# Kernel optimization log

Hardware: AMD Instinct MI355X
Metric: run time of the kernel (lower is better)

## Reference

```python
import jax, jax.numpy as jnp
import numpy as np

D_MODEL = 1024
N_HEADS = 8
D_HEAD = 64
D_FF = 4096
LAMBDA_INIT = 0.8
EPS = 1e-5


def _ln(x, g, b):
    m = jnp.mean(x, axis=-1, keepdims=True)
    v = jnp.mean(jnp.square(x - m), axis=-1, keepdims=True)
    return (x - m) * jax.lax.rsqrt(v + EPS) * g + b


def setup_inputs() -> dict:
    key = jax.random.key(0)
    ks = jax.random.split(key, 24)
    D, H, Dh, F = D_MODEL, N_HEADS, D_HEAD, D_FF
    P = 2 * H * Dh  # projection width for q/k/v (== D here)
    s = lambda fan: 1.0 / np.sqrt(fan)
    inp = {
        'x': jax.random.normal(ks[0], (2, 2048, D), jnp.float32),
        'ln1_g': jnp.ones((D,), jnp.float32), 'ln1_b': jnp.zeros((D,), jnp.float32),
        'ln2_g': jnp.ones((D,), jnp.float32), 'ln2_b': jnp.zeros((D,), jnp.float32),
        'Wq': jax.random.normal(ks[1], (D, P), jnp.float32) * s(D), 'bq': jnp.zeros((P,), jnp.float32),
        'Wk': jax.random.normal(ks[2], (D, P), jnp.float32) * s(D), 'bk': jnp.zeros((P,), jnp.float32),
        'Wv': jax.random.normal(ks[3], (D, P), jnp.float32) * s(D), 'bv': jnp.zeros((P,), jnp.float32),
        'Wo': jax.random.normal(ks[4], (P, D), jnp.float32) * s(P), 'bo': jnp.zeros((D,), jnp.float32),
        'lq1': jax.random.normal(ks[5], (H, Dh), jnp.float32) * 0.1,
        'lk1': jax.random.normal(ks[6], (H, Dh), jnp.float32) * 0.1,
        'lq2': jax.random.normal(ks[7], (H, Dh), jnp.float32) * 0.1,
        'lk2': jax.random.normal(ks[8], (H, Dh), jnp.float32) * 0.1,
        'gn_w': jnp.ones((P,), jnp.float32), 'gn_b': jnp.zeros((P,), jnp.float32),
        'W1': jax.random.normal(ks[9], (D, F), jnp.float32) * s(D), 'b1': jnp.zeros((F,), jnp.float32),
        'Wg': jax.random.normal(ks[10], (F, F), jnp.float32) * s(F), 'bg': jnp.zeros((F,), jnp.float32),
        'W2': jax.random.normal(ks[11], (F, D), jnp.float32) * s(F), 'b2': jnp.zeros((D,), jnp.float32),
    }
    return inp


def reference(x, ln1_g, ln1_b, ln2_g, ln2_b, Wq, bq, Wk, bk, Wv, bv, Wo, bo,
              lq1, lk1, lq2, lk2, gn_w, gn_b, W1, b1, Wg, bg, W2, b2):
    B, S, D = x.shape
    H, Dh = N_HEADS, D_HEAD
    scale = 1.0 / np.sqrt(Dh)

    # --- differential attention sublayer (pre-norm) ---
    h = _ln(x, ln1_g, ln1_b)
    q = (h @ Wq + bq).reshape(B, S, H, 2, Dh)
    k = (h @ Wk + bk).reshape(B, S, H, 2, Dh)
    v = (h @ Wv + bv).reshape(B, S, H, 2 * Dh)

    A1 = jax.nn.softmax(jnp.einsum('bshd,bthd->bhst', q[..., 0, :], k[..., 0, :]) * scale, axis=-1)
    A2 = jax.nn.softmax(jnp.einsum('bshd,bthd->bhst', q[..., 1, :], k[..., 1, :]) * scale, axis=-1)

    lam = (jnp.exp(jnp.sum(lq1 * lk1, axis=-1))
           - jnp.exp(jnp.sum(lq2 * lk2, axis=-1)) + LAMBDA_INIT)  # [H]
    diff = A1 - lam[None, :, None, None] * A2                     # [B,H,S,S]
    o = jnp.einsum('bhst,bthe->bshe', diff, v)                    # [B,S,H,2*Dh]

    # headwise GroupNorm over the 2*Dh channels of each head
    mu = jnp.mean(o, axis=-1, keepdims=True)
    var = jnp.mean(jnp.square(o - mu), axis=-1, keepdims=True)
    o = (o - mu) * jax.lax.rsqrt(var + EPS)
    o = o * gn_w.reshape(H, 2 * Dh) + gn_b.reshape(H, 2 * Dh)
    o = o * (1.0 - LAMBDA_INIT)

    attn_out = o.reshape(B, S, 2 * H * Dh) @ Wo + bo
    x = x + attn_out

    # --- FFN sublayer: note source applies prenorm2 BEFORE residual split ---
    x = _ln(x, ln2_g, ln2_b)
    u = x @ W1 + b1
    u = u * jax.nn.silu(u @ Wg + bg)   # swiGLU gate
    return x + (u @ W2 + b2)
```

## Files before the change

kernel.cpp:

```cpp
#include <hip/hip_runtime.h>
#include <hip/hip_bf16.h>


typedef __attribute__((ext_vector_type(8))) __bf16 bf16x8;
typedef __attribute__((ext_vector_type(4))) float f32x4;

#define GAS __attribute__((address_space(1)))
#define LAS __attribute__((address_space(3)))

__device__ __forceinline__ unsigned short f2bf(float f) {
  unsigned u = __float_as_uint(f);
  u += 0x7fffu + ((u >> 16) & 1u);
  return (unsigned short)(u >> 16);
}
__device__ __forceinline__ float bf2f(unsigned short s) {
  return __uint_as_float(((unsigned)s) << 16);
}

__global__ __launch_bounds__(256)
void transpose_cvt(const float* __restrict__ W, unsigned short* __restrict__ WT,
                   int K, int N, float scale) {
  __shared__ float tile[64][65];
  const int n0 = blockIdx.x * 64, k0 = blockIdx.y * 64;
  const int tr = threadIdx.x >> 4, tc = (threadIdx.x & 15) * 4;
#pragma unroll
  for (int i = 0; i < 4; ++i) {
    const float4 v = *(const float4*)&W[(size_t)(k0 + tr + i * 16) * N + n0 + tc];
    tile[tr + i * 16][tc + 0] = v.x;
    tile[tr + i * 16][tc + 1] = v.y;
    tile[tr + i * 16][tc + 2] = v.z;
    tile[tr + i * 16][tc + 3] = v.w;
  }
  __syncthreads();
#pragma unroll
  for (int i = 0; i < 4; ++i) {
    const int n = tr + i * 16;
    ushort4 o;
    o.x = f2bf(tile[tc + 0][n] * scale);
    o.y = f2bf(tile[tc + 1][n] * scale);
    o.z = f2bf(tile[tc + 2][n] * scale);
    o.w = f2bf(tile[tc + 3][n] * scale);
    *(ushort4*)&WT[(size_t)(n0 + n) * K + k0 + tc] = o;
  }
}

__global__ void prep_bias(const float* __restrict__ bq, const float* __restrict__ bk,
                          const float* __restrict__ bv, float* __restrict__ out,
                          float qscale) {
  const int i = blockIdx.x * 256 + threadIdx.x;
  if (i < 1024) out[i] = bq[i] * qscale;
  else if (i < 2048) out[i] = bk[i - 1024];
  else out[i] = bv[i - 2048];
}

__global__ __launch_bounds__(256)
void k_pack(const unsigned short* __restrict__ qkv, unsigned short* __restrict__ KP) {
  const int bh = blockIdx.y, b = bh >> 3, h = bh & 7;
  const int s0 = blockIdx.x * 16;
  const int sl = threadIdx.x >> 4, e8 = (threadIdx.x & 15) * 8;
  const size_t src = (size_t)b * 2048 * 3072 + (size_t)(s0 + sl) * 3072 + 1024 + h * 128 + e8;
  const size_t dst = ((size_t)bh * 2048 + s0 + sl) * 128 + e8;
  *(uint4*)&KP[dst] = *(const uint4*)&qkv[src];
}

__global__ __launch_bounds__(256)
void v_transpose(const unsigned short* __restrict__ v, unsigned short* __restrict__ VT) {
  __shared__ unsigned short tile[64][65];
  const int s0 = blockIdx.x * 64, e0 = blockIdx.y * 64, bh = blockIdx.z;
  const int b = bh >> 3, h = bh & 7;
  const int tr = threadIdx.x >> 4, tc = (threadIdx.x & 15) * 4;
  const size_t inbase = (size_t)b * 2048 * 3072 + h * 128;
#pragma unroll
  for (int i = 0; i < 4; ++i) {
    const int r = tr + i * 16;
    const ushort4 val = *(const ushort4*)&v[inbase + (size_t)(s0 + r) * 3072 + e0 + tc];
    tile[r][tc + 0] = val.x;
    tile[r][tc + 1] = val.y;
    tile[r][tc + 2] = val.z;
    tile[r][tc + 3] = val.w;
  }
  __syncthreads();
#pragma unroll
  for (int i = 0; i < 4; ++i) {
    const int n = tr + i * 16;
    ushort4 oo;
    oo.x = tile[tc + 0][n];
    oo.y = tile[tc + 1][n];
    oo.z = tile[tc + 2][n];
    oo.w = tile[tc + 3][n];
    *(ushort4*)&VT[(size_t)(bh * 128 + e0 + n) * 2048 + s0 + tc] = oo;
  }
}

__global__ void lam_kernel(const float* __restrict__ lq1, const float* __restrict__ lk1,
                           const float* __restrict__ lq2, const float* __restrict__ lk2,
                           float* __restrict__ lam) {
  const int w = threadIdx.x >> 6, d = threadIdx.x & 63;
  float a = lq1[w * 64 + d] * lk1[w * 64 + d];
  float c = lq2[w * 64 + d] * lk2[w * 64 + d];
#pragma unroll
  for (int off = 32; off; off >>= 1) {
    a += __shfl_xor(a, off);
    c += __shfl_xor(c, off);
  }
  if (d == 0) lam[w] = __expf(a) - __expf(c) + 0.8f;
}

template <int WRITE_F32>
__global__ __launch_bounds__(256)
void ln_kernel(const float* __restrict__ x, const float* __restrict__ g,
               const float* __restrict__ bsh, unsigned short* __restrict__ obf,
               float* __restrict__ of32) {
  __shared__ float red[16];
  const int row = blockIdx.x, tid = threadIdx.x;
  const float4 v = *(const float4*)&x[(size_t)row * 1024 + tid * 4];
  float s = v.x + v.y + v.z + v.w;
  float q = v.x * v.x + v.y * v.y + v.z * v.z + v.w * v.w;
#pragma unroll
  for (int off = 32; off; off >>= 1) {
    s += __shfl_xor(s, off);
    q += __shfl_xor(q, off);
  }
  if ((tid & 63) == 0) {
    red[tid >> 6] = s;
    red[8 + (tid >> 6)] = q;
  }
  __syncthreads();
  s = red[0] + red[1] + red[2] + red[3];
  q = red[8] + red[9] + red[10] + red[11];
  const float mean = s * (1.f / 1024.f);
  const float var = q * (1.f / 1024.f) - mean * mean;
  const float rstd = rsqrtf(var + 1e-5f);
  const float4 gg = *(const float4*)&g[tid * 4];
  const float4 bb = *(const float4*)&bsh[tid * 4];
  float y0 = (v.x - mean) * rstd * gg.x + bb.x;
  float y1 = (v.y - mean) * rstd * gg.y + bb.y;
  float y2 = (v.z - mean) * rstd * gg.z + bb.z;
  float y3 = (v.w - mean) * rstd * gg.w + bb.w;
  const size_t base = (size_t)row * 1024 + tid * 4;
  ushort4 o;
  o.x = f2bf(y0); o.y = f2bf(y1); o.z = f2bf(y2); o.w = f2bf(y3);
  *(ushort4*)&obf[base] = o;
  if (WRITE_F32) {
    *(float4*)&of32[base] = make_float4(y0, y1, y2, y3);
  }
}

template <int EPI>
__global__ __launch_bounds__(256)
void gemm_n64(const unsigned short* __restrict__ A,
              const unsigned short* __restrict__ BT,
              const float* __restrict__ bias,
              const float* __restrict__ res,
              void* __restrict__ Cout, int M, int N, int K, float bscale) {
  __shared__ unsigned short ldsA[2][128 * 32];
  __shared__ unsigned short ldsB[2][64 * 32];
  const int tid = threadIdx.x;
  const int wv = tid >> 6, ln = tid & 63, lg = ln >> 4, lc = ln & 15;
  const int wm = wv >> 1, wn = wv & 1;
  const int nwg = gridDim.x * gridDim.y;
  const int linear = blockIdx.y * gridDim.x + blockIdx.x;
  const int swz = (linear & 7) * (nwg >> 3) + (linear >> 3);
  const int m0 = (swz / gridDim.x) * 128, n0 = (swz % gridDim.x) * 64;
  const int rsub = ln >> 2;
  const int sw_inner = ((ln & 3) * 16) ^ ((rsub & 3) << 4);
  const int acol = sw_inner >> 1;

  f32x4 acc[4][2];
#pragma unroll
  for (int i = 0; i < 4; ++i)
#pragma unroll
    for (int j = 0; j < 2; ++j) acc[i][j] = (f32x4)0.f;

  auto stage = [&](int buf, int k0) {
#pragma unroll
    for (int j = 0; j < 2; ++j) {
      const int rowblk = wv * 32 + j * 16;
      const unsigned short* ga = A + (size_t)(m0 + rowblk + rsub) * K + (k0 + acol);
      __builtin_amdgcn_global_load_lds((GAS void*)ga,
          (LAS void*)&ldsA[buf][rowblk * 32], 16, 0, 0);
    }
    const unsigned short* gb = BT + (size_t)(n0 + wv * 16 + rsub) * K + (k0 + acol);
    __builtin_amdgcn_global_load_lds((GAS void*)gb,
        (LAS void*)&ldsB[buf][wv * 16 * 32], 16, 0, 0);
  };

  const int nk = K / 32;
  stage(0, 0);
  int cur = 0;
  for (int i = 0; i < nk; ++i) {
    if (i + 1 < nk) {
      stage(cur ^ 1, (i + 1) * 32);
      asm volatile("s_waitcnt vmcnt(3)" ::: "memory");
    } else {
      asm volatile("s_waitcnt vmcnt(0)" ::: "memory");
    }
    __builtin_amdgcn_s_barrier();
    bf16x8 af[4], bf[2];
#pragma unroll
    for (int m = 0; m < 4; ++m) {
      const int r = wm * 64 + m * 16 + lc;
      af[m] = *(const bf16x8*)((const char*)&ldsA[cur][0] + r * 64 +
                               ((lg * 16) ^ ((r & 3) << 4)));
    }
#pragma unroll
    for (int n = 0; n < 2; ++n) {
      const int r = wn * 32 + n * 16 + lc;
      bf[n] = *(const bf16x8*)((const char*)&ldsB[cur][0] + r * 64 +
                               ((lg * 16) ^ ((r & 3) << 4)));
    }
    __builtin_amdgcn_s_setprio(1);
#pragma unroll
    for (int m = 0; m < 4; ++m)
#pragma unroll
      for (int n = 0; n < 2; ++n)
        acc[m][n] = __builtin_amdgcn_mfma_f32_16x16x32_bf16(af[m], bf[n], acc[m][n], 0, 0, 0);
    __builtin_amdgcn_s_setprio(0);
    __builtin_amdgcn_s_barrier();
    cur ^= 1;
  }

#pragma unroll
  for (int m = 0; m < 4; ++m) {
#pragma unroll
    for (int n = 0; n < 2; ++n) {
      const int c = n0 + wn * 32 + n * 16 + lc;
      const float bc = bias[c] * bscale;
#pragma unroll
      for (int j = 0; j < 4; ++j) {
        const int r = m0 + wm * 64 + m * 16 + lg * 4 + j;
        const size_t idx = (size_t)r * N + c;
        const float v = acc[m][n][j] + bc;
        if (EPI == 1) {
          ((float*)Cout)[idx] = res[idx] + v;
        } else {
          ((unsigned short*)Cout)[idx] = f2bf(v);
        }
      }
    }
  }
}

template <int EPI>
__global__ __launch_bounds__(512)
void gemm256(const unsigned short* __restrict__ A,
             const unsigned short* __restrict__ BT,
             const float* __restrict__ bias,
             const unsigned short* __restrict__ gate_u,
             unsigned short* __restrict__ Cout, int M, int N, int K) {
  __shared__ unsigned short lds[65536];
  const int tid = threadIdx.x;
  const int w = tid >> 6, ln = tid & 63, lg = ln >> 4, lc = ln & 15;
  const int wm = w >> 2, wn = w & 3;
  const int nwg = gridDim.x * gridDim.y;
  const int linear = blockIdx.y * gridDim.x + blockIdx.x;
  const int swzb = (linear & 7) * (nwg >> 3) + (linear >> 3);
  const int m0 = (swzb / gridDim.x) * 256, n0 = (swzb % gridDim.x) * 256;

  f32x4 acc[8][4];
#pragma unroll
  for (int i = 0; i < 8; ++i)
#pragma unroll
    for (int j = 0; j < 4; ++j) acc[i][j] = (f32x4)0.f;

  auto stage_half = [&](int tensor, int j, int hh) {
    const unsigned short* base = tensor ? BT : A;
    const int row0 = (tensor ? n0 : m0) + hh * 128;
    const int slot = tensor * 4 + (j & 1) * 2 + hh;
#pragma unroll
    for (int c = 0; c < 2; ++c) {
      const int chunk = w * 2 + c;
      const int L = chunk * 1024 + ln * 16;
      const int r = L >> 7, inner = L & 127;
      const char* src = (const char*)(base + (size_t)(row0 + r) * K + j * 64) +
                        (inner ^ ((r & 7) << 4));
      __builtin_amdgcn_global_load_lds((GAS void*)src,
          (LAS void*)((char*)lds + slot * 16384 + chunk * 1024), 16, 0, 0);
    }
  };
  auto read_a = [&](int j, int mf, int ks) -> bf16x8 {
    const int r = mf * 16 + lc;
    const int slot = (j & 1) * 2 + wm;
    const int cb = ks * 64 + lg * 16;
    return *(const bf16x8*)((const char*)lds + slot * 16384 + r * 128 +
                            (cb ^ ((r & 7) << 4)));
  };
  auto read_b = [&](int j, int nf, int ks) -> bf16x8 {
    const int R = wn * 64 + nf * 16 + lc;
    const int slot = 4 + (j & 1) * 2 + (R >> 7);
    const int r = R & 127;
    const int cb = ks * 64 + lg * 16;
    return *(const bf16x8*)((const char*)lds + slot * 16384 + r * 128 +
                            (cb ^ ((r & 7) << 4)));
  };

  const int nkt = K / 64;

  stage_half(0, 0, 0); stage_half(0, 0, 1);
  stage_half(1, 0, 0); stage_half(1, 0, 1);
  stage_half(1, 1, 0); stage_half(1, 1, 1);
  asm volatile("s_waitcnt vmcnt(0)" ::: "memory");
  __builtin_amdgcn_s_barrier();

  bf16x8 bfr[4][2];
  for (int it = 0; it < nkt / 2; ++it) {
    const int J = it * 2;
#pragma unroll
    for (int half = 0; half < 2; ++half) {
      const int jc = J + half;
#pragma unroll
      for (int q = 0; q < 4; ++q) {
        if (q == 0) {
#pragma unroll
          for (int nf = 0; nf < 4; ++nf)
#pragma unroll
            for (int ks = 0; ks < 2; ++ks) bfr[nf][ks] = read_b(jc, nf, ks);
        }
        bf16x8 afr[2][2];
#pragma unroll
        for (int mm = 0; mm < 2; ++mm)
#pragma unroll
          for (int ks = 0; ks < 2; ++ks) afr[mm][ks] = read_a(jc, q * 2 + mm, ks);
        if (half == 0) {
          if (q == 0) stage_half(0, J + 1, 0);
          if (q == 1) stage_half(0, J + 1, 1);
          if (q == 2 && J + 2 < nkt) stage_half(1, J + 2, 0);
          if (q == 3 && J + 2 < nkt) stage_half(1, J + 2, 1);
        } else {
          if (q == 0 && J + 2 < nkt) stage_half(0, J + 2, 0);
          if (q == 1 && J + 2 < nkt) stage_half(0, J + 2, 1);
          if (q == 2 && J + 3 < nkt) stage_half(1, J + 3, 0);
          if (q == 3 && J + 3 < nkt) stage_half(1, J + 3, 1);
        }
        if (q == 0) asm volatile("s_waitcnt lgkmcnt(8)" ::: "memory");
        __builtin_amdgcn_s_barrier();
        __builtin_amdgcn_s_setprio(1);
#pragma unroll
        for (int mm = 0; mm < 2; ++mm)
#pragma unroll
          for (int nf = 0; nf < 4; ++nf)
#pragma unroll
            for (int ks = 0; ks < 2; ++ks)
              acc[q * 2 + mm][nf] = __builtin_amdgcn_mfma_f32_16x16x32_bf16(
                  afr[mm][ks], bfr[nf][ks], acc[q * 2 + mm][nf], 0, 0, 0);
        __builtin_amdgcn_s_setprio(0);
        if (q == 3) asm volatile("s_waitcnt vmcnt(4)" ::: "memory");
        __builtin_amdgcn_s_barrier();
      }
    }
  }

#pragma unroll
  for (int mf = 0; mf < 8; ++mf) {
#pragma unroll
    for (int nf = 0; nf < 4; ++nf) {
      const int c = n0 + wn * 64 + nf * 16 + lc;
      const float bc = bias[c];
#pragma unroll
      for (int jj = 0; jj < 4; ++jj) {
        const int r = m0 + wm * 128 + mf * 16 + lg * 4 + jj;
        const size_t idx = (size_t)r * N + c;
        const float v = acc[mf][nf][jj] + bc;
        if (EPI == 0) {
          Cout[idx] = f2bf(v);
        } else {
          const float uu = bf2f(gate_u[idx]);
          const float sw = v / (1.f + __expf(-v));
          Cout[idx] = f2bf(uu * sw);
        }
      }
    }
  }
}

__global__ __launch_bounds__(256)
void attn_kernel(const unsigned short* __restrict__ q,
                 const unsigned short* __restrict__ KP,
                 const unsigned short* __restrict__ VT,
                 const float* __restrict__ lam,
                 const float* __restrict__ gn_w, const float* __restrict__ gn_b,
                 unsigned short* __restrict__ o) {
  constexpr int S = 2048;
  constexpr int QS = 3072;
  __shared__ unsigned short k_tile[2][32 * 128];
  __shared__ unsigned short v_tile[2][128 * 32];
  __shared__ unsigned short p_lds[4][2][512];
  const int tid = threadIdx.x, w = tid >> 6, ln = tid & 63, lg = ln >> 4, lc = ln & 15;
  const int id = blockIdx.x;
  const int bh = (id & 7) + 8 * ((id >> 8) & 1);
  const int qt = (id >> 3) & 31;
  const int h = bh & 7, b = bh >> 3;
  const size_t chan = (size_t)b * S * QS + h * 128;
  const size_t ochan = (size_t)b * S * 1024 + h * 128;
  const size_t kpbase = (size_t)bh * S * 128;
  const size_t vtbase = (size_t)bh * 128 * S;
  const int qrow = qt * 64 + w * 16 + lc;

  bf16x8 qf[2][2];
#pragma unroll
  for (int p = 0; p < 2; ++p)
#pragma unroll
    for (int ks = 0; ks < 2; ++ks)
      qf[p][ks] = *(const bf16x8*)&q[chan + (size_t)qrow * QS + p * 64 + ks * 32 + lg * 8];

  f32x4 O[2][8];
#pragma unroll
  for (int p = 0; p < 2; ++p)
#pragma unroll
    for (int ef = 0; ef < 8; ++ef) O[p][ef] = (f32x4)0.f;
  float lsum[2][4];
#pragma unroll
  for (int p = 0; p < 2; ++p)
#pragma unroll
    for (int j = 0; j < 4; ++j) lsum[p][j] = 0.f;

  const int prd = ((lc * 64 + lg * 16) ^ ((lc & 7) << 4)) >> 1;

  auto stage = [&](int buf, int t0) {
#pragma unroll
    for (int c = 0; c < 2; ++c) {
      {
        const int L = (w * 2 + c) * 1024 + ln * 16;
        const int r = L >> 8, inner = L & 255;
        const char* src = (const char*)(KP + kpbase + (size_t)(t0 + r) * 128) +
                          (inner ^ ((r & 7) << 4));
        __builtin_amdgcn_global_load_lds((GAS void*)src,
            (LAS void*)((char*)&k_tile[buf][0] + (w * 2 + c) * 1024), 16, 0, 0);
      }
      {
        const int L = (w * 2 + c) * 1024 + ln * 16;
        const int e = L >> 6, inner = L & 63;
        const char* src = (const char*)(VT + vtbase + (size_t)e * S + t0) +
                          (inner ^ ((e & 3) << 4));
        __builtin_amdgcn_global_load_lds((GAS void*)src,
            (LAS void*)((char*)&v_tile[buf][0] + (w * 2 + c) * 1024), 16, 0, 0);
      }
    }
  };

  auto compute = [&](int buf) {
    const char* kb = (const char*)&k_tile[buf][0];
    const char* vb = (const char*)&v_tile[buf][0];
    bf16x8 vf[8];
#pragma unroll
    for (int ef = 0; ef < 8; ++ef) {
      const int e = ef * 16 + lc;
      vf[ef] = *(const bf16x8*)(vb + e * 64 + ((lg * 16) ^ ((e & 3) << 4)));
    }
#pragma unroll
    for (int p = 0; p < 2; ++p) {
      bf16x8 kf[2][2];
#pragma unroll
      for (int tf = 0; tf < 2; ++tf) {
        const int r = tf * 16 + lc;
#pragma unroll
        for (int ks = 0; ks < 2; ++ks)
          kf[tf][ks] = *(const bf16x8*)(kb + r * 256 +
                          ((p * 128 + ks * 64 + lg * 16) ^ ((r & 7) << 4)));
      }
      f32x4 sfr[2];
      __builtin_amdgcn_s_setprio(1);
#pragma unroll
      for (int tf = 0; tf < 2; ++tf) {
        f32x4 acc = (f32x4)0.f;
#pragma unroll
        for (int ks = 0; ks < 2; ++ks)
          acc = __builtin_amdgcn_mfma_f32_16x16x32_bf16(qf[p][ks], kf[tf][ks], acc, 0, 0, 0);
        sfr[tf] = acc;
      }
      __builtin_amdgcn_s_setprio(0);

#pragma unroll
      for (int tf = 0; tf < 2; ++tf)
#pragma unroll
        for (int j = 0; j < 4; ++j) {
          const float e = __expf(sfr[tf][j]);
          lsum[p][j] += e;
          const int qq = lg * 4 + j;
          const int wi = ((qq * 64 + (tf * 16 + lc) * 2) ^ ((qq & 7) << 4)) >> 1;
          p_lds[w][p][wi] = f2bf(e);
        }

      const bf16x8 pa = *(const bf16x8*)&p_lds[w][p][prd];
      __builtin_amdgcn_s_setprio(1);
#pragma unroll
      for (int ef = 0; ef < 8; ++ef)
        O[p][ef] = __builtin_amdgcn_mfma_f32_16x16x32_bf16(pa, vf[ef], O[p][ef], 0, 0, 0);
      __builtin_amdgcn_s_setprio(0);
    }
  };

  stage(0, 0);
  int cur = 0;
  for (int it = 0; it < 64; ++it) {
    if (it < 63) {
      stage(cur ^ 1, (it + 1) * 32);
      asm volatile("s_waitcnt vmcnt(4)" ::: "memory");
    } else {
      asm volatile("s_waitcnt vmcnt(0)" ::: "memory");
    }
    __builtin_amdgcn_s_barrier();
    compute(cur);
    __builtin_amdgcn_s_barrier();
    cur ^= 1;
  }

#pragma unroll
  for (int p = 0; p < 2; ++p)
#pragma unroll
    for (int j = 0; j < 4; ++j) {
      float s = lsum[p][j];
      s += __shfl_xor(s, 1);
      s += __shfl_xor(s, 2);
      s += __shfl_xor(s, 4);
      s += __shfl_xor(s, 8);
      lsum[p][j] = s;
    }
  const float lamh = lam[h];
#pragma unroll
  for (int j = 0; j < 4; ++j) {
    const float inv1 = 1.f / lsum[0][j];
    const float inv2 = lamh / lsum[1][j];
    float dv[8], sum = 0.f, sq = 0.f;
#pragma unroll
    for (int ef = 0; ef < 8; ++ef) {
      dv[ef] = O[0][ef][j] * inv1 - O[1][ef][j] * inv2;
      sum += dv[ef];
      sq += dv[ef] * dv[ef];
    }
    sum += __shfl_xor(sum, 1); sq += __shfl_xor(sq, 1);
    sum += __shfl_xor(sum, 2); sq += __shfl_xor(sq, 2);
    sum += __shfl_xor(sum, 4); sq += __shfl_xor(sq, 4);
    sum += __shfl_xor(sum, 8); sq += __shfl_xor(sq, 8);
    const float mean = sum * (1.f / 128.f);
    const float var = sq * (1.f / 128.f) - mean * mean;
    const float rstd = rsqrtf(var + 1e-5f);
    const int row = qt * 64 + w * 16 + lg * 4 + j;
#pragma unroll
    for (int ef = 0; ef < 8; ++ef) {
      const int e = ef * 16 + lc;
      const float val = (dv[ef] - mean) * rstd * gn_w[h * 128 + e] + gn_b[h * 128 + e];
      o[ochan + (size_t)row * 1024 + e] = f2bf(val * 0.2f);
    }
  }
}

extern "C" void kernel_launch(void* const* d_in, const int* in_sizes, int n_in,
                              void* d_out, int out_size, void* d_ws, size_t ws_size,
                              hipStream_t stream) {
  (void)in_sizes; (void)n_in; (void)out_size; (void)ws_size;
  const float* x    = (const float*)d_in[0];
  const float* ln1g = (const float*)d_in[1];
  const float* ln1b = (const float*)d_in[2];
  const float* ln2g = (const float*)d_in[3];
  const float* ln2b = (const float*)d_in[4];
  const float* Wq   = (const float*)d_in[5];
  const float* bq   = (const float*)d_in[6];
  const float* Wk   = (const float*)d_in[7];
  const float* bk   = (const float*)d_in[8];
  const float* Wv   = (const float*)d_in[9];
  const float* bv   = (const float*)d_in[10];
  const float* Wo   = (const float*)d_in[11];
  const float* bo   = (const float*)d_in[12];
  const float* lq1  = (const float*)d_in[13];
  const float* lk1  = (const float*)d_in[14];
  const float* lq2  = (const float*)d_in[15];
  const float* lk2  = (const float*)d_in[16];
  const float* gnw  = (const float*)d_in[17];
  const float* gnb  = (const float*)d_in[18];
  const float* W1   = (const float*)d_in[19];
  const float* b1   = (const float*)d_in[20];
  const float* Wg   = (const float*)d_in[21];
  const float* bg   = (const float*)d_in[22];
  const float* W2   = (const float*)d_in[23];
  const float* b2   = (const float*)d_in[24];

  const int B = 2, S = 2048, D = 1024, F = 4096;
  const int M = B * S;
  const float qscale = 0.125f;

  char* ws = (char*)d_ws;
  size_t off = 0;
  auto alloc = [&](size_t bytes) {
    char* p = ws + off;
    off += (bytes + 255) & ~(size_t)255;
    return p;
  };
  unsigned short* WqkvT = (unsigned short*)alloc((size_t)3 * D * D * 2);
  unsigned short* WoT = (unsigned short*)alloc((size_t)D * D * 2);
  unsigned short* W1T = (unsigned short*)alloc((size_t)F * D * 2);
  unsigned short* WgT = (unsigned short*)alloc((size_t)F * F * 2);
  unsigned short* W2T = (unsigned short*)alloc((size_t)D * F * 2);
  float*          lamw= (float*)alloc(256);
  float*          bqkv= (float*)alloc(3072 * 4);
  unsigned short* h_bf= (unsigned short*)alloc((size_t)M * D * 2);
  unsigned short* qkv = (unsigned short*)alloc((size_t)M * 3 * D * 2);
  unsigned short* o_bf= (unsigned short*)alloc((size_t)M * D * 2);
  float*          x1  = (float*)alloc((size_t)M * D * 4);
  float*          x2  = (float*)alloc((size_t)M * D * 4);
  unsigned short* x2b = (unsigned short*)alloc((size_t)M * D * 2);
  unsigned short* u_bf= (unsigned short*)alloc((size_t)M * F * 2);
  unsigned short* w_bf= h_bf;

  unsigned short* KP = (unsigned short*)x1;
  unsigned short* VT = u_bf + (size_t)12 * 1024 * 1024;

  transpose_cvt<<<dim3(D / 64, D / 64), 256, 0, stream>>>(Wq, WqkvT, D, D, qscale);
  transpose_cvt<<<dim3(D / 64, D / 64), 256, 0, stream>>>(Wk, WqkvT + (size_t)D * D, D, D, 1.0f);
  transpose_cvt<<<dim3(D / 64, D / 64), 256, 0, stream>>>(Wv, WqkvT + (size_t)2 * D * D, D, D, 1.0f);
  transpose_cvt<<<dim3(D / 64, D / 64), 256, 0, stream>>>(Wo, WoT, D, D, 1.0f);
  transpose_cvt<<<dim3(F / 64, D / 64), 256, 0, stream>>>(W1, W1T, D, F, 1.0f);
  transpose_cvt<<<dim3(F / 64, F / 64), 256, 0, stream>>>(Wg, WgT, F, F, 1.0f);
  transpose_cvt<<<dim3(D / 64, F / 64), 256, 0, stream>>>(W2, W2T, F, D, 1.0f);
  prep_bias<<<12, 256, 0, stream>>>(bq, bk, bv, bqkv, qscale);
  lam_kernel<<<1, 512, 0, stream>>>(lq1, lk1, lq2, lk2, lamw);

  ln_kernel<0><<<M, 256, 0, stream>>>(x, ln1g, ln1b, h_bf, nullptr);
  gemm256<0><<<dim3(3 * D / 256, M / 256), 512, 0, stream>>>(h_bf, WqkvT, bqkv, nullptr, qkv, M, 3 * D, D);
  k_pack<<<dim3(S / 16, 16), 256, 0, stream>>>(qkv, KP);
  v_transpose<<<dim3(S / 64, 2, 16), 256, 0, stream>>>(qkv + 2048, VT);
  attn_kernel<<<dim3(512), 256, 0, stream>>>(qkv, KP, VT, lamw, gnw, gnb, o_bf);
  gemm_n64<1><<<dim3(D / 64, M / 128), 256, 0, stream>>>(o_bf, WoT, bo, x, x1, M, D, D, 1.0f);

  ln_kernel<1><<<M, 256, 0, stream>>>(x1, ln2g, ln2b, x2b, x2);
  gemm256<0><<<dim3(F / 256, M / 256), 512, 0, stream>>>(x2b, W1T, b1, nullptr, u_bf, M, F, D);
  gemm256<2><<<dim3(F / 256, M / 256), 512, 0, stream>>>(u_bf, WgT, bg, u_bf, w_bf, M, F, F);
  gemm_n64<1><<<dim3(D / 64, M / 128), 256, 0, stream>>>(w_bf, W2T, b2, x2, (float*)d_out, M, D, F, 1.0f);
}
```

Before: 451.6 us.

## Fuse K pack and V transpose, drop fp32 LN2 output, tune attention occupancy

Merges the K packing and V transpose kernels into one kv_prep launch that reads each QKV tile once. The second LayerNorm no longer writes an fp32 copy, and the final GEMM takes its residual from the bf16 normalized activations instead. This removes a launch and about 16MB of fp32 write and read traffic. It costs residual precision, because the final output now adds a bf16-rounded residual, and it adds launch_bounds(256,4) on the attention kernel, which may force register spills.

```diff
diff --git a/kernel.cpp b/kernel.cpp
--- a/kernel.cpp
+++ b/kernel.cpp
@@ -54,41 +54,38 @@
 }
 
 __global__ __launch_bounds__(256)
-void k_pack(const unsigned short* __restrict__ qkv, unsigned short* __restrict__ KP) {
+void kv_prep(const unsigned short* __restrict__ qkv, unsigned short* __restrict__ KP,
+             unsigned short* __restrict__ VT) {
+  __shared__ unsigned short tile[128][66];
   const int bh = blockIdx.y, b = bh >> 3, h = bh & 7;
-  const int s0 = blockIdx.x * 16;
-  const int sl = threadIdx.x >> 4, e8 = (threadIdx.x & 15) * 8;
-  const size_t src = (size_t)b * 2048 * 3072 + (size_t)(s0 + sl) * 3072 + 1024 + h * 128 + e8;
-  const size_t dst = ((size_t)bh * 2048 + s0 + sl) * 128 + e8;
-  *(uint4*)&KP[dst] = *(const uint4*)&qkv[src];
-}
-
-__global__ __launch_bounds__(256)
-void v_transpose(const unsigned short* __restrict__ v, unsigned short* __restrict__ VT) {
-  __shared__ unsigned short tile[64][65];
-  const int s0 = blockIdx.x * 64, e0 = blockIdx.y * 64, bh = blockIdx.z;
-  const int b = bh >> 3, h = bh & 7;
-  const int tr = threadIdx.x >> 4, tc = (threadIdx.x & 15) * 4;
+  const int s0 = blockIdx.x * 64;
   const size_t inbase = (size_t)b * 2048 * 3072 + h * 128;
+  const int tr = threadIdx.x >> 4, tc = (threadIdx.x & 15) * 8;
+#pragma unroll
+  for (int i = 0; i < 4; ++i) {
+    const int s = s0 + tr + i * 16;
+    *(uint4*)&KP[((size_t)bh * 2048 + s) * 128 + tc] =
+        *(const uint4*)&qkv[inbase + (size_t)s * 3072 + 1024 + tc];
+  }
 #pragma unroll
   for (int i = 0; i < 4; ++i) {
     const int r = tr + i * 16;
-    const ushort4 val = *(const ushort4*)&v[inbase + (size_t)(s0 + r) * 3072 + e0 + tc];
-    tile[r][tc + 0] = val.x;
-    tile[r][tc + 1] = val.y;
-    tile[r][tc + 2] = val.z;
-    tile[r][tc + 3] = val.w;
+    const uint4 v = *(const uint4*)&qkv[inbase + (size_t)(s0 + r) * 3072 + 2048 + tc];
+    const unsigned short* pv = (const unsigned short*)&v;
+#pragma unroll
+    for (int jj = 0; jj < 8; ++jj) tile[tc + jj][r] = pv[jj];
   }
   __syncthreads();
+  const int e = threadIdx.x >> 1, sh = (threadIdx.x & 1) * 32;
 #pragma unroll
   for (int i = 0; i < 4; ++i) {
-    const int n = tr + i * 16;
-    ushort4 oo;
-    oo.x = tile[tc + 0][n];
-    oo.y = tile[tc + 1][n];
-    oo.z = tile[tc + 2][n];
-    oo.w = tile[tc + 3][n];
-    *(ushort4*)&VT[(size_t)(bh * 128 + e0 + n) * 2048 + s0 + tc] = oo;
+    ushort4 o0, o1;
+    o0.x = tile[e][sh + i * 8 + 0]; o0.y = tile[e][sh + i * 8 + 1];
+    o0.z = tile[e][sh + i * 8 + 2]; o0.w = tile[e][sh + i * 8 + 3];
+    o1.x = tile[e][sh + i * 8 + 4]; o1.y = tile[e][sh + i * 8 + 5];
+    o1.z = tile[e][sh + i * 8 + 6]; o1.w = tile[e][sh + i * 8 + 7];
+    *(ushort4*)&VT[((size_t)bh * 128 + e) * 2048 + s0 + sh + i * 8] = o0;
+    *(ushort4*)&VT[((size_t)bh * 128 + e) * 2048 + s0 + sh + i * 8 + 4] = o1;
   }
 }
 
@@ -106,11 +103,9 @@
   if (d == 0) lam[w] = __expf(a) - __expf(c) + 0.8f;
 }
 
-template <int WRITE_F32>
 __global__ __launch_bounds__(256)
 void ln_kernel(const float* __restrict__ x, const float* __restrict__ g,
-               const float* __restrict__ bsh, unsigned short* __restrict__ obf,
-               float* __restrict__ of32) {
+               const float* __restrict__ bsh, unsigned short* __restrict__ obf) {
   __shared__ float red[16];
   const int row = blockIdx.x, tid = threadIdx.x;
   const float4 v = *(const float4*)&x[(size_t)row * 1024 + tid * 4];
@@ -133,17 +128,12 @@
   const float rstd = rsqrtf(var + 1e-5f);
   const float4 gg = *(const float4*)&g[tid * 4];
   const float4 bb = *(const float4*)&bsh[tid * 4];
-  float y0 = (v.x - mean) * rstd * gg.x + bb.x;
-  float y1 = (v.y - mean) * rstd * gg.y + bb.y;
-  float y2 = (v.z - mean) * rstd * gg.z + bb.z;
-  float y3 = (v.w - mean) * rstd * gg.w + bb.w;
-  const size_t base = (size_t)row * 1024 + tid * 4;
   ushort4 o;
-  o.x = f2bf(y0); o.y = f2bf(y1); o.z = f2bf(y2); o.w = f2bf(y3);
-  *(ushort4*)&obf[base] = o;
-  if (WRITE_F32) {
-    *(float4*)&of32[base] = make_float4(y0, y1, y2, y3);
-  }
+  o.x = f2bf((v.x - mean) * rstd * gg.x + bb.x);
+  o.y = f2bf((v.y - mean) * rstd * gg.y + bb.y);
+  o.z = f2bf((v.z - mean) * rstd * gg.z + bb.z);
+  o.w = f2bf((v.w - mean) * rstd * gg.w + bb.w);
+  *(ushort4*)&obf[(size_t)row * 1024 + tid * 4] = o;
 }
 
 template <int EPI>
@@ -151,7 +141,8 @@
 void gemm_n64(const unsigned short* __restrict__ A,
               const unsigned short* __restrict__ BT,
               const float* __restrict__ bias,
-              const float* __restrict__ res,
+              const float* __restrict__ resf,
+              const unsigned short* __restrict__ resb,
               void* __restrict__ Cout, int M, int N, int K, float bscale) {
   __shared__ unsigned short ldsA[2][128 * 32];
   __shared__ unsigned short ldsB[2][64 * 32];
@@ -232,7 +223,9 @@
         const size_t idx = (size_t)r * N + c;
         const float v = acc[m][n][j] + bc;
         if (EPI == 1) {
-          ((float*)Cout)[idx] = res[idx] + v;
+          ((float*)Cout)[idx] = resf[idx] + v;
+        } else if (EPI == 2) {
+          ((float*)Cout)[idx] = bf2f(resb[idx]) + v;
         } else {
           ((unsigned short*)Cout)[idx] = f2bf(v);
         }
@@ -373,7 +366,7 @@
   }
 }
 
-__global__ __launch_bounds__(256)
+__global__ __launch_bounds__(256, 4)
 void attn_kernel(const unsigned short* __restrict__ q,
                  const unsigned short* __restrict__ KP,
                  const unsigned short* __restrict__ VT,
@@ -597,7 +590,6 @@
   unsigned short* qkv = (unsigned short*)alloc((size_t)M * 3 * D * 2);
   unsigned short* o_bf= (unsigned short*)alloc((size_t)M * D * 2);
   float*          x1  = (float*)alloc((size_t)M * D * 4);
-  float*          x2  = (float*)alloc((size_t)M * D * 4);
   unsigned short* x2b = (unsigned short*)alloc((size_t)M * D * 2);
   unsigned short* u_bf= (unsigned short*)alloc((size_t)M * F * 2);
   unsigned short* w_bf= h_bf;
@@ -615,15 +607,14 @@
   prep_bias<<<12, 256, 0, stream>>>(bq, bk, bv, bqkv, qscale);
   lam_kernel<<<1, 512, 0, stream>>>(lq1, lk1, lq2, lk2, lamw);
 
-  ln_kernel<0><<<M, 256, 0, stream>>>(x, ln1g, ln1b, h_bf, nullptr);
+  ln_kernel<<<M, 256, 0, stream>>>(x, ln1g, ln1b, h_bf);
   gemm256<0><<<dim3(3 * D / 256, M / 256), 512, 0, stream>>>(h_bf, WqkvT, bqkv, nullptr, qkv, M, 3 * D, D);
-  k_pack<<<dim3(S / 16, 16), 256, 0, stream>>>(qkv, KP);
-  v_transpose<<<dim3(S / 64, 2, 16), 256, 0, stream>>>(qkv + 2048, VT);
+  kv_prep<<<dim3(S / 64, 16), 256, 0, stream>>>(qkv, KP, VT);
   attn_kernel<<<dim3(512), 256, 0, stream>>>(qkv, KP, VT, lamw, gnw, gnb, o_bf);
-  gemm_n64<1><<<dim3(D / 64, M / 128), 256, 0, stream>>>(o_bf, WoT, bo, x, x1, M, D, D, 1.0f);
-
-  ln_kernel<1><<<M, 256, 0, stream>>>(x1, ln2g, ln2b, x2b, x2);
+  gemm_n64<1><<<dim3(D / 64, M / 128), 256, 0, stream>>>(o_bf, WoT, bo, x, nullptr, x1, M, D, D, 1.0f);
+
+  ln_kernel<<<M, 256, 0, stream>>>(x1, ln2g, ln2b, x2b);
   gemm256<0><<<dim3(F / 256, M / 256), 512, 0, stream>>>(x2b, W1T, b1, nullptr, u_bf, M, F, D);
   gemm256<2><<<dim3(F / 256, M / 256), 512, 0, stream>>>(u_bf, WgT, bg, u_bf, w_bf, M, F, F);
-  gemm_n64<1><<<dim3(D / 64, M / 128), 256, 0, stream>>>(w_bf, W2T, b2, x2, (float*)d_out, M, D, F, 1.0f);
-}
+  gemm_n64<2><<<dim3(D / 64, M / 128), 256, 0, stream>>>(w_bf, W2T, b2, nullptr, x2b, (float*)d_out, M, D, F, 1.0f);
+}
```

Result: slower. 735.1 us (+62.8%).
